# Kernel tuning notes

Hardware: AMD Instinct MI355X
Metric: run time of the kernel (lower is better)

The kernel has to match this reference:

```python
import jax, jax.numpy as jnp
import numpy as np

B = 4096          # number of sessions
MEAN_LEN = 50     # mean items per session
N = B * MEAN_LEN  # total items (ragged lengths sum to this)
H = 256           # feat_input_dim == context_input_dim == hidden_dim


def setup_inputs() -> dict:
    key = jax.random.key(0)
    k1, k2, k3, k4, k5, k6, k7 = jax.random.split(key, 7)
    # ragged lengths in [20, 80] adjusted so they sum exactly to N
    rng = np.random.default_rng(0)
    lens = rng.integers(20, 81, size=B)
    lens = (lens * (N / lens.sum())).astype(np.int64)
    lens[-1] += N - lens.sum()
    s = 1.0 / np.sqrt(H)
    return {
        "feats": jax.random.normal(k1, (N, H), jnp.float32),
        "feat_context": jax.random.normal(k2, (N, H), jnp.float32),
        "batch_num_items": jnp.asarray(lens, jnp.int64),
        "Wu": jax.random.uniform(k3, (H, H), jnp.float32, -s, s),
        "bu": jax.random.uniform(k4, (H,), jnp.float32, -s, s),
        "Wv": jax.random.uniform(k5, (H, H), jnp.float32, -s, s),
        "We": jax.random.uniform(k6, (H,), jnp.float32, -s, s),
        "Wout": jax.random.uniform(k7, (H, H), jnp.float32, -s, s),
    }


def reference(feats, feat_context, batch_num_items, Wu, bu, Wv, We, Wout):
    n = feats.shape[0]
    b = batch_num_items.shape[0]
    # additive attention score per item
    feat_u = feats @ Wu.T + bu                     # [N, H]
    feat_v = feat_context @ Wv.T                   # [N, H]
    e = jax.nn.sigmoid(feat_u + feat_v) @ We       # [N]
    # segment ids from ragged lengths (static total length => jit-safe)
    seg = jnp.repeat(jnp.arange(b), batch_num_items, total_repeat_length=n)
    # segment softmax (numerically stable)
    m = jax.ops.segment_max(e, seg, num_segments=b)        # [B]
    ex = jnp.exp(e - m[seg])                               # [N]
    denom = jax.ops.segment_sum(ex, seg, num_segments=b)   # [B]
    alpha = ex / denom[seg]                                # [N]
    # weighted segment-sum pooling
    rst = jax.ops.segment_sum(feats * alpha[:, None], seg, num_segments=b)  # [B, H]
    return rst @ Wout.T
```

## Files before the change

### kernel.cpp

```cpp
#include <hip/hip_runtime.h>
#include <hip/hip_bf16.h>
#include <cstdint>
#include <cstddef>

#define H 256
#define CHUNK 128

typedef __attribute__((ext_vector_type(8))) short    frag8;
typedef __attribute__((ext_vector_type(4))) float    f32x4;
typedef __attribute__((ext_vector_type(4))) uint32_t u32x4;
typedef __attribute__((ext_vector_type(8))) unsigned short ushort8;

__device__ __forceinline__ unsigned short f32_to_bf16(float f) {
    uint32_t u = __float_as_uint(f);
    u = (u + 0x7FFFu + ((u >> 16) & 1u)) >> 16;
    return (unsigned short)u;
}

__device__ __forceinline__ uint32_t pk_bf16(float a, float b) {
    union { __hip_bfloat162 h2; uint32_t u; } cv;
    cv.h2 = __float22bfloat162_rn(make_float2(a, b));
    return cv.u;
}

__global__ void prep(const float* __restrict__ Wu, const float* __restrict__ Wv,
                     const float* __restrict__ Wout,
                     unsigned short* __restrict__ Wopt, float* __restrict__ WoutT) {
    int bid = blockIdx.x, tid = threadIdx.x;
    if (bid < 64) {
        int idx  = bid * 256 + tid;
        int lane = idx & 63;
        int ct   = (idx >> 6) & 15;
        int ksg  = idx >> 10;
        int col  = ct * 16 + (lane & 15);
        int kg   = ksg * 32 + (lane >> 4) * 8;
        ushort8 pk;
        #pragma unroll
        for (int j = 0; j < 8; j++) {
            int k = kg + j;
            float v = (k < 256) ? Wu[col * 256 + k] : Wv[col * 256 + (k - 256)];
            pk[j] = f32_to_bf16(v);
        }
        *(ushort8*)&Wopt[(size_t)idx * 8] = pk;
    } else {
        int t2 = (bid - 64) * 256 + tid;
        int j = t2 & 255, k = t2 >> 8;
        WoutT[t2] = Wout[j * 256 + k];
    }
}

__global__ void seg_offsets(const int* __restrict__ lens, int B, int* __restrict__ off,
                            int2* __restrict__ chunks, int* __restrict__ chunk_cnt) {
    __shared__ int partL[256], partC[256];
    int tid = threadIdx.x;
    bool is64 = (B >= 3) && (lens[1] == 0) && (lens[3] == 0) && (lens[5] == 0);
    int per = (B + 255) / 256;
    int base = tid * per;
    int sL = 0, sC = 0;
    for (int i = 0; i < per; i++) {
        int idx = base + i;
        if (idx < B) {
            int l = is64 ? lens[2 * idx] : lens[idx];
            sL += l;
            sC += (l + CHUNK - 1) / CHUNK;
        }
    }
    partL[tid] = sL; partC[tid] = sC;
    __syncthreads();
    for (int d = 1; d < 256; d <<= 1) {
        int vL = partL[tid], vC = partC[tid];
        int aL = (tid >= d) ? partL[tid - d] : 0;
        int aC = (tid >= d) ? partC[tid - d] : 0;
        __syncthreads();
        partL[tid] = vL + aL; partC[tid] = vC + aC;
        __syncthreads();
    }
    int runL = partL[tid] - sL;
    int runC = partC[tid] - sC;
    for (int i = 0; i < per; i++) {
        int idx = base + i;
        if (idx < B) {
            int l = is64 ? lens[2 * idx] : lens[idx];
            off[idx] = runL;
            int n = (l + CHUNK - 1) / CHUNK;
            for (int c = 0; c < n; c++)
                chunks[runC + c] = make_int2(idx, runL + c * CHUNK);
            runC += n;
            runL += l;
        }
    }
    if (tid == 255) { off[B] = partL[255]; chunk_cnt[0] = partC[255]; }
}

__global__ __launch_bounds__(256) void fused_e(
        const float* __restrict__ feats, const float* __restrict__ ctx,
        const unsigned short* __restrict__ Wopt,
        const float* __restrict__ bu, const float* __restrict__ We,
        float* __restrict__ e_out) {
    __shared__ unsigned short a_lds[64 * 128];
    __shared__ float e_part[4 * 64];

    const int tid  = threadIdx.x;
    const int lane = tid & 63;
    const int w    = tid >> 6;
    const int l15  = lane & 15;
    const int q    = lane >> 4;
    const size_t m0 = (size_t)blockIdx.x * 64;
    const int r0   = tid >> 3;
    const int c8   = tid & 7;
    const int swz  = r0 & 15;

    f32x4 acc[4][4];
    #pragma unroll
    for (int i = 0; i < 4; i++)
        #pragma unroll
        for (int j = 0; j < 4; j++)
            acc[i][j] = (f32x4)(0.0f);

    f32x4 pre[8];
    {
        const float* pA = feats + (m0 + r0) * H + c8 * 16;
        const float* pB = feats + (m0 + r0 + 32) * H + c8 * 16;
        pre[0] = *(const f32x4*)pA;       pre[1] = *(const f32x4*)(pA + 4);
        pre[2] = *(const f32x4*)(pA + 8); pre[3] = *(const f32x4*)(pA + 12);
        pre[4] = *(const f32x4*)pB;       pre[5] = *(const f32x4*)(pB + 4);
        pre[6] = *(const f32x4*)(pB + 8); pre[7] = *(const f32x4*)(pB + 12);
    }

    #pragma unroll
    for (int kt = 0; kt < 4; ++kt) {
        u32x4 g0, g1, g2, g3;
        g0[0] = pk_bf16(pre[0][0], pre[0][1]); g0[1] = pk_bf16(pre[0][2], pre[0][3]);
        g0[2] = pk_bf16(pre[1][0], pre[1][1]); g0[3] = pk_bf16(pre[1][2], pre[1][3]);
        g1[0] = pk_bf16(pre[2][0], pre[2][1]); g1[1] = pk_bf16(pre[2][2], pre[2][3]);
        g1[2] = pk_bf16(pre[3][0], pre[3][1]); g1[3] = pk_bf16(pre[3][2], pre[3][3]);
        g2[0] = pk_bf16(pre[4][0], pre[4][1]); g2[1] = pk_bf16(pre[4][2], pre[4][3]);
        g2[2] = pk_bf16(pre[5][0], pre[5][1]); g2[3] = pk_bf16(pre[5][2], pre[5][3]);
        g3[0] = pk_bf16(pre[6][0], pre[6][1]); g3[1] = pk_bf16(pre[6][2], pre[6][3]);
        g3[2] = pk_bf16(pre[7][0], pre[7][1]); g3[3] = pk_bf16(pre[7][2], pre[7][3]);

        __syncthreads();
        *(u32x4*)&a_lds[ r0       * 128 + (((2 * c8    ) ^ swz) * 8)] = g0;
        *(u32x4*)&a_lds[ r0       * 128 + (((2 * c8 + 1) ^ swz) * 8)] = g1;
        *(u32x4*)&a_lds[(r0 + 32) * 128 + (((2 * c8    ) ^ swz) * 8)] = g2;
        *(u32x4*)&a_lds[(r0 + 32) * 128 + (((2 * c8 + 1) ^ swz) * 8)] = g3;
        __syncthreads();

        if (kt < 3) {
            const float* src = (kt + 1 < 2) ? feats : ctx;
            const int kb = ((kt + 1) & 1) * 128;
            const float* pA = src + (m0 + r0) * H + kb + c8 * 16;
            const float* pB = src + (m0 + r0 + 32) * H + kb + c8 * 16;
            pre[0] = *(const f32x4*)pA;       pre[1] = *(const f32x4*)(pA + 4);
            pre[2] = *(const f32x4*)(pA + 8); pre[3] = *(const f32x4*)(pA + 12);
            pre[4] = *(const f32x4*)pB;       pre[5] = *(const f32x4*)(pB + 4);
            pre[6] = *(const f32x4*)(pB + 8); pre[7] = *(const f32x4*)(pB + 12);
        }

        #pragma unroll
        for (int ks = 0; ks < 4; ++ks) {
            const int ksg = kt * 4 + ks;
            frag8 afr[4], bfr[4];
            #pragma unroll
            for (int ci = 0; ci < 4; ++ci)
                bfr[ci] = *(const frag8*)&Wopt[(((size_t)ksg * 16 + w * 4 + ci) * 64 + lane) * 8];
            #pragma unroll
            for (int rt = 0; rt < 4; ++rt)
                afr[rt] = *(const frag8*)&a_lds[(rt * 16 + l15) * 128 + (((ks * 4 + q) ^ l15) * 8)];
            #pragma unroll
            for (int rt = 0; rt < 4; ++rt)
                #pragma unroll
                for (int ci = 0; ci < 4; ++ci)
                    acc[rt][ci] = __builtin_amdgcn_mfma_f32_16x16x32_bf16(
                        afr[rt], bfr[ci], acc[rt][ci], 0, 0, 0);
        }
    }

    float buv[4], wev[4];
    #pragma unroll
    for (int ci = 0; ci < 4; ++ci) {
        int col = w * 64 + ci * 16 + l15;
        buv[ci] = bu[col];
        wev[ci] = We[col];
    }
    #pragma unroll
    for (int rt = 0; rt < 4; ++rt) {
        #pragma unroll
        for (int r = 0; r < 4; ++r) {
            float s = 0.0f;
            #pragma unroll
            for (int ci = 0; ci < 4; ++ci) {
                float h = acc[rt][ci][r] + buv[ci];
                s += wev[ci] * __builtin_amdgcn_rcpf(1.0f + __expf(-h));
            }
            s += __shfl_xor(s, 1, 64);
            s += __shfl_xor(s, 2, 64);
            s += __shfl_xor(s, 4, 64);
            s += __shfl_xor(s, 8, 64);
            if (l15 == 0) e_part[w * 64 + rt * 16 + q * 4 + r] = s;
        }
    }
    __syncthreads();
    if (tid < 64)
        e_out[m0 + tid] = e_part[tid] + e_part[64 + tid] + e_part[128 + tid] + e_part[192 + tid];
}

__global__ __launch_bounds__(256) void seg_stats(
        float* __restrict__ e, const int* __restrict__ off, int B) {
    int seg = blockIdx.x * 4 + (threadIdx.x >> 6);
    int lane = threadIdx.x & 63;
    if (seg >= B) return;
    int start = off[seg];
    int len = off[seg + 1] - start;
    float m = -3.0e38f;
    for (int i = lane; i < len; i += 64) m = fmaxf(m, e[start + i]);
    #pragma unroll
    for (int o = 32; o > 0; o >>= 1) m = fmaxf(m, __shfl_xor(m, o, 64));
    float s = 0.0f;
    for (int i = lane; i < len; i += 64) s += __expf(e[start + i] - m);
    #pragma unroll
    for (int o = 32; o > 0; o >>= 1) s += __shfl_xor(s, o, 64);
    float inv = (s > 0.0f) ? 1.0f / s : 0.0f;
    for (int i = lane; i < len; i += 64) e[start + i] = __expf(e[start + i] - m) * inv;
}

__global__ __launch_bounds__(256) void pool_chunks(
        const float* __restrict__ alpha, const float* __restrict__ feats,
        const int* __restrict__ off, const int2* __restrict__ chunks,
        const int* __restrict__ chunk_cnt, float* __restrict__ rst) {
    __shared__ float redf[4 * 256];
    int idx = blockIdx.x;
    if (idx >= chunk_cnt[0]) return;
    int2 en = chunks[idx];
    int seg = en.x, cstart = en.y;
    int sstart = off[seg], send = off[seg + 1];
    int clen = send - cstart;
    if (clen > CHUNK) clen = CHUNK;
    int tid = threadIdx.x, lane = tid & 63, g = tid >> 6;

    const f32x4* F = (const f32x4*)feats + (size_t)cstart * 64 + lane;
    const float* A = alpha + cstart;
    f32x4 acc0 = (f32x4)(0.0f), acc1 = (f32x4)(0.0f);
    int i = g;
    for (; i + 4 < clen; i += 8) {
        acc0 += A[i]     * F[(size_t)i * 64];
        acc1 += A[i + 4] * F[(size_t)(i + 4) * 64];
    }
    if (i < clen) acc0 += A[i] * F[(size_t)i * 64];
    acc0 += acc1;
    *(f32x4*)&redf[g * 256 + lane * 4] = acc0;
    __syncthreads();
    float v = redf[tid] + redf[256 + tid] + redf[512 + tid] + redf[768 + tid];
    if (send - sstart > CHUNK) atomicAdd(&rst[(size_t)seg * H + tid], v);
    else rst[(size_t)seg * H + tid] = v;
}

#define RB 8
__global__ __launch_bounds__(256) void out_gemm(
        const float* __restrict__ rst, const float* __restrict__ WoutT,
        float* __restrict__ out) {
    __shared__ float r[RB * 256];
    const int tid = threadIdx.x;
    const size_t b0 = (size_t)blockIdx.x * RB;
    for (int i = tid; i < RB * 256; i += 256) r[i] = rst[b0 * 256 + i];
    __syncthreads();
    float acc[RB];
    #pragma unroll
    for (int j = 0; j < RB; j++) acc[j] = 0.0f;
    for (int k = 0; k < 256; k += 4) {
        f32x4 rw[RB];
        #pragma unroll
        for (int j = 0; j < RB; j++) rw[j] = *(const f32x4*)&r[j * 256 + k];
        #pragma unroll
        for (int kk = 0; kk < 4; kk++) {
            float wv = WoutT[(size_t)(k + kk) * 256 + tid];
            #pragma unroll
            for (int j = 0; j < RB; j++) acc[j] += rw[j][kk] * wv;
        }
    }
    #pragma unroll
    for (int j = 0; j < RB; j++) out[(b0 + j) * 256 + tid] = acc[j];
}

extern "C" void kernel_launch(void* const* d_in, const int* in_sizes, int n_in,
                              void* d_out, int out_size, void* d_ws, size_t ws_size,
                              hipStream_t stream) {
    const float* feats = (const float*)d_in[0];
    const float* ctx   = (const float*)d_in[1];
    const int*   lens  = (const int*)d_in[2];
    const float* Wu    = (const float*)d_in[3];
    const float* bu    = (const float*)d_in[4];
    const float* Wv    = (const float*)d_in[5];
    const float* We    = (const float*)d_in[6];
    const float* Wout  = (const float*)d_in[7];
    float* out = (float*)d_out;

    const int N = in_sizes[0] / H;
    const int B = in_sizes[2];
    const int maxChunks = B + (N + CHUNK - 1) / CHUNK;

    char* w = (char*)d_ws;
    auto carve = [&](size_t bytes) {
        char* p = w;
        w += (bytes + 255) & ~(size_t)255;
        return p;
    };
    int*            off    = (int*)           carve((size_t)(B + 1) * sizeof(int));
    float*          e      = (float*)         carve((size_t)N * sizeof(float));
    float*          rst    = (float*)         carve((size_t)B * H * sizeof(float));
    unsigned short* Wopt   = (unsigned short*)carve((size_t)16 * 16 * 64 * 8 * sizeof(unsigned short));
    float*          WoutT  = (float*)         carve((size_t)H * H * sizeof(float));
    int2*           chunks = (int2*)          carve((size_t)maxChunks * sizeof(int2));
    int*            ccnt   = (int*)           carve(sizeof(int));

    hipMemsetAsync(rst, 0, (size_t)B * H * sizeof(float), stream);

    prep        <<<320,         256, 0, stream>>>(Wu, Wv, Wout, Wopt, WoutT);
    seg_offsets <<<1,           256, 0, stream>>>(lens, B, off, chunks, ccnt);
    fused_e     <<<N / 64,      256, 0, stream>>>(feats, ctx, Wopt, bu, We, e);
    seg_stats   <<<(B + 3) / 4, 256, 0, stream>>>(e, off, B);
    pool_chunks <<<maxChunks,   256, 0, stream>>>(e, feats, off, chunks, ccnt, rst);
    out_gemm    <<<B / RB,      256, 0, stream>>>(rst, WoutT, out);
}
```

Baseline: 537.6 us.

## Split fused_e across 8 waves with 32 columns each and hoist B-fragment loads

The fused score kernel now runs 512 threads per block (8 waves), and each wave covers 32 output columns instead of 64. Per-thread accumulator and prefetch registers are halved, and each thread stages one row of the A tile instead of two. All four k-step weight fragments for a k-tile are loaded up front, ahead of the global prefetch, with a sched_barrier between them. The goal is more waves in flight to hide load latency, at the cost of an 8-way partial-sum reduction and more barrier participants per block.

```diff
diff --git a/kernel.cpp b/kernel.cpp
--- a/kernel.cpp
+++ b/kernel.cpp
@@ -92,13 +92,13 @@
     if (tid == 255) { off[B] = partL[255]; chunk_cnt[0] = partC[255]; }
 }
 
-__global__ __launch_bounds__(256) void fused_e(
+__global__ __launch_bounds__(512, 4) void fused_e(
         const float* __restrict__ feats, const float* __restrict__ ctx,
         const unsigned short* __restrict__ Wopt,
         const float* __restrict__ bu, const float* __restrict__ We,
         float* __restrict__ e_out) {
     __shared__ unsigned short a_lds[64 * 128];
-    __shared__ float e_part[4 * 64];
+    __shared__ float e_part[8 * 64];
 
     const int tid  = threadIdx.x;
     const int lane = tid & 63;
@@ -110,76 +110,69 @@
     const int c8   = tid & 7;
     const int swz  = r0 & 15;
 
-    f32x4 acc[4][4];
+    f32x4 acc[4][2];
     #pragma unroll
     for (int i = 0; i < 4; i++)
         #pragma unroll
-        for (int j = 0; j < 4; j++)
+        for (int j = 0; j < 2; j++)
             acc[i][j] = (f32x4)(0.0f);
 
-    f32x4 pre[8];
+    f32x4 pre[4];
     {
-        const float* pA = feats + (m0 + r0) * H + c8 * 16;
-        const float* pB = feats + (m0 + r0 + 32) * H + c8 * 16;
-        pre[0] = *(const f32x4*)pA;       pre[1] = *(const f32x4*)(pA + 4);
-        pre[2] = *(const f32x4*)(pA + 8); pre[3] = *(const f32x4*)(pA + 12);
-        pre[4] = *(const f32x4*)pB;       pre[5] = *(const f32x4*)(pB + 4);
-        pre[6] = *(const f32x4*)(pB + 8); pre[7] = *(const f32x4*)(pB + 12);
+        const float* p = feats + (m0 + r0) * H + c8 * 16;
+        pre[0] = *(const f32x4*)p;       pre[1] = *(const f32x4*)(p + 4);
+        pre[2] = *(const f32x4*)(p + 8); pre[3] = *(const f32x4*)(p + 12);
     }
 
     #pragma unroll
     for (int kt = 0; kt < 4; ++kt) {
-        u32x4 g0, g1, g2, g3;
+        u32x4 g0, g1;
         g0[0] = pk_bf16(pre[0][0], pre[0][1]); g0[1] = pk_bf16(pre[0][2], pre[0][3]);
         g0[2] = pk_bf16(pre[1][0], pre[1][1]); g0[3] = pk_bf16(pre[1][2], pre[1][3]);
         g1[0] = pk_bf16(pre[2][0], pre[2][1]); g1[1] = pk_bf16(pre[2][2], pre[2][3]);
         g1[2] = pk_bf16(pre[3][0], pre[3][1]); g1[3] = pk_bf16(pre[3][2], pre[3][3]);
-        g2[0] = pk_bf16(pre[4][0], pre[4][1]); g2[1] = pk_bf16(pre[4][2], pre[4][3]);
-        g2[2] = pk_bf16(pre[5][0], pre[5][1]); g2[3] = pk_bf16(pre[5][2], pre[5][3]);
-        g3[0] = pk_bf16(pre[6][0], pre[6][1]); g3[1] = pk_bf16(pre[6][2], pre[6][3]);
-        g3[2] = pk_bf16(pre[7][0], pre[7][1]); g3[3] = pk_bf16(pre[7][2], pre[7][3]);
 
         __syncthreads();
-        *(u32x4*)&a_lds[ r0       * 128 + (((2 * c8    ) ^ swz) * 8)] = g0;
-        *(u32x4*)&a_lds[ r0       * 128 + (((2 * c8 + 1) ^ swz) * 8)] = g1;
-        *(u32x4*)&a_lds[(r0 + 32) * 128 + (((2 * c8    ) ^ swz) * 8)] = g2;
-        *(u32x4*)&a_lds[(r0 + 32) * 128 + (((2 * c8 + 1) ^ swz) * 8)] = g3;
+        *(u32x4*)&a_lds[r0 * 128 + (((2 * c8    ) ^ swz) * 8)] = g0;
+        *(u32x4*)&a_lds[r0 * 128 + (((2 * c8 + 1) ^ swz) * 8)] = g1;
         __syncthreads();
+
+        frag8 bfr[4][2];
+        #pragma unroll
+        for (int ks = 0; ks < 4; ++ks)
+            #pragma unroll
+            for (int ci = 0; ci < 2; ++ci)
+                bfr[ks][ci] = *(const frag8*)&Wopt[
+                    (((size_t)(kt * 4 + ks) * 16 + (w * 2 + ci)) * 64 + lane) * 8];
+        __builtin_amdgcn_sched_barrier(0);
 
         if (kt < 3) {
             const float* src = (kt + 1 < 2) ? feats : ctx;
             const int kb = ((kt + 1) & 1) * 128;
-            const float* pA = src + (m0 + r0) * H + kb + c8 * 16;
-            const float* pB = src + (m0 + r0 + 32) * H + kb + c8 * 16;
-            pre[0] = *(const f32x4*)pA;       pre[1] = *(const f32x4*)(pA + 4);
-            pre[2] = *(const f32x4*)(pA + 8); pre[3] = *(const f32x4*)(pA + 12);
-            pre[4] = *(const f32x4*)pB;       pre[5] = *(const f32x4*)(pB + 4);
-            pre[6] = *(const f32x4*)(pB + 8); pre[7] = *(const f32x4*)(pB + 12);
+            const float* p = src + (m0 + r0) * H + kb + c8 * 16;
+            pre[0] = *(const f32x4*)p;       pre[1] = *(const f32x4*)(p + 4);
+            pre[2] = *(const f32x4*)(p + 8); pre[3] = *(const f32x4*)(p + 12);
         }
 
         #pragma unroll
         for (int ks = 0; ks < 4; ++ks) {
-            const int ksg = kt * 4 + ks;
-            frag8 afr[4], bfr[4];
-            #pragma unroll
-            for (int ci = 0; ci < 4; ++ci)
-                bfr[ci] = *(const frag8*)&Wopt[(((size_t)ksg * 16 + w * 4 + ci) * 64 + lane) * 8];
+            frag8 afr[4];
             #pragma unroll
             for (int rt = 0; rt < 4; ++rt)
                 afr[rt] = *(const frag8*)&a_lds[(rt * 16 + l15) * 128 + (((ks * 4 + q) ^ l15) * 8)];
             #pragma unroll
             for (int rt = 0; rt < 4; ++rt)
                 #pragma unroll
-                for (int ci = 0; ci < 4; ++ci)
+                for (int ci = 0; ci < 2; ++ci)
                     acc[rt][ci] = __builtin_amdgcn_mfma_f32_16x16x32_bf16(
-                        afr[rt], bfr[ci], acc[rt][ci], 0, 0, 0);
-        }
-    }
-
-    float buv[4], wev[4];
-    #pragma unroll
-    for (int ci = 0; ci < 4; ++ci) {
-        int col = w * 64 + ci * 16 + l15;
+                        afr[rt], bfr[ks][ci], acc[rt][ci], 0, 0, 0);
+        }
+    }
+
+    float buv[2], wev[2];
+    #pragma unroll
+    for (int ci = 0; ci < 2; ++ci) {
+        int col = w * 32 + ci * 16 + l15;
         buv[ci] = bu[col];
         wev[ci] = We[col];
     }
@@ -189,7 +182,7 @@
         for (int r = 0; r < 4; ++r) {
             float s = 0.0f;
             #pragma unroll
-            for (int ci = 0; ci < 4; ++ci) {
+            for (int ci = 0; ci < 2; ++ci) {
                 float h = acc[rt][ci][r] + buv[ci];
                 s += wev[ci] * __builtin_amdgcn_rcpf(1.0f + __expf(-h));
             }
@@ -201,8 +194,12 @@
         }
     }
     __syncthreads();
-    if (tid < 64)
-        e_out[m0 + tid] = e_part[tid] + e_part[64 + tid] + e_part[128 + tid] + e_part[192 + tid];
+    if (tid < 64) {
+        float s = 0.0f;
+        #pragma unroll
+        for (int ww = 0; ww < 8; ++ww) s += e_part[ww * 64 + tid];
+        e_out[m0 + tid] = s;
+    }
 }
 
 __global__ __launch_bounds__(256) void seg_stats(
@@ -317,7 +314,7 @@
 
     prep        <<<320,         256, 0, stream>>>(Wu, Wv, Wout, Wopt, WoutT);
     seg_offsets <<<1,           256, 0, stream>>>(lens, B, off, chunks, ccnt);
-    fused_e     <<<N / 64,      256, 0, stream>>>(feats, ctx, Wopt, bu, We, e);
+    fused_e     <<<N / 64,      512, 0, stream>>>(feats, ctx, Wopt, bu, We, e);
     seg_stats   <<<(B + 3) / 4, 256, 0, stream>>>(e, off, B);
     pool_chunks <<<maxChunks,   256, 0, stream>>>(e, feats, off, chunks, ccnt, rst);
     out_gemm    <<<B / RB,      256, 0, stream>>>(rst, WoutT, out);
```

Result: faster. 525.4 us (-2.3%).
